# Performance work log

Measured on AMD Instinct MI355X. Metric: run time of the kernel, lower is better.

The kernel has to match this reference:

```python
import jax, jax.numpy as jnp
import numpy as np

N, E, F_IN, HID, HEADS, NCLS = 50000, 800000, 500, 16, 8, 40
NEG_SLOPE = 0.2


def setup_inputs() -> dict:
    key = jax.random.key(0)
    ks = jax.random.split(key, 10)
    x = jax.random.normal(ks[0], (N, F_IN), jnp.float32)
    edge_index = jax.random.randint(ks[1], (2, E), 0, N)
    W1 = jax.random.normal(ks[2], (F_IN, HEADS * HID), jnp.float32) * (1.0 / np.sqrt(F_IN))
    a_src1 = jax.random.normal(ks[3], (HEADS, HID), jnp.float32) * 0.1
    a_dst1 = jax.random.normal(ks[4], (HEADS, HID), jnp.float32) * 0.1
    b1 = jnp.zeros((HEADS * HID,), jnp.float32)
    W2 = jax.random.normal(ks[5], (HEADS * HID, NCLS), jnp.float32) * (1.0 / np.sqrt(HEADS * HID))
    a_src2 = jax.random.normal(ks[6], (1, NCLS), jnp.float32) * 0.1
    a_dst2 = jax.random.normal(ks[7], (1, NCLS), jnp.float32) * 0.1
    b2 = jnp.zeros((NCLS,), jnp.float32)
    return {"x": x, "edge_index": edge_index, "W1": W1, "a_src1": a_src1,
            "a_dst1": a_dst1, "b1": b1, "W2": W2, "a_src2": a_src2,
            "a_dst2": a_dst2, "b2": b2}


def gat_layer(x, edge_index, W, a_src, a_dst, b, heads, ch, concat):
    n = x.shape[0]
    h = (x @ W).reshape(n, heads, ch)                 # [N,H,C]
    alpha_src = jnp.sum(h * a_src, axis=-1)           # [N,H]
    alpha_dst = jnp.sum(h * a_dst, axis=-1)           # [N,H]
    loop = jnp.arange(n)                              # PyG add_self_loops=True
    src = jnp.concatenate([edge_index[0], loop])
    dst = jnp.concatenate([edge_index[1], loop])
    e = jax.nn.leaky_relu(alpha_src[src] + alpha_dst[dst], NEG_SLOPE)  # [E',H]
    # segment softmax over destination nodes
    m = jax.ops.segment_max(e, dst, num_segments=n)
    ex = jnp.exp(e - m[dst])
    denom = jax.ops.segment_sum(ex, dst, num_segments=n)
    alpha = ex / (denom[dst] + 1e-16)                 # [E',H]
    out = jax.ops.segment_sum(h[src] * alpha[:, :, None], dst, num_segments=n)  # [N,H,C]
    out = out.reshape(n, heads * ch) if concat else out.mean(axis=1)
    return out + b


def reference(x, edge_index, W1, a_src1, a_dst1, b1, W2, a_src2, a_dst2, b2):
    h = jax.nn.elu(gat_layer(x, edge_index, W1, a_src1, a_dst1, b1, HEADS, HID, True))
    # dropout p=0.6 is identity in eval mode
    h = gat_layer(h, edge_index, W2, a_src2, a_dst2, b2, 1, NCLS, False)
    return jax.nn.log_softmax(h, axis=1)
```

## Files before the change

### kernel.cpp

```cpp
#include <hip/hip_runtime.h>
#include <hip/hip_bf16.h>
#include <math.h>

#define N_NODES 50000
#define F_IN    500
#define HEADS   8
#define HID     16
#define HH      128
#define NCLS    40
#define NEG     0.2f

typedef _Float16 f16x2 __attribute__((ext_vector_type(2)));
typedef _Float16 f16x4 __attribute__((ext_vector_type(4)));
typedef _Float16 f16x8 __attribute__((ext_vector_type(8)));
typedef float    f32x4 __attribute__((ext_vector_type(4)));

__device__ __forceinline__ float lrelu(float x) { return x >= 0.f ? x : NEG * x; }

__global__ void convW_kernel(const float* __restrict__ W1, _Float16* __restrict__ Wt) {
    int i = blockIdx.x * 256 + threadIdx.x;
    if (i >= 128 * 512) return;
    int c = i >> 9, k = i & 511;
    Wt[i] = (k < F_IN) ? (_Float16)W1[k * HH + c] : (_Float16)0.f;
}

#define LDPB 136
__global__ __launch_bounds__(256) void gemm1_mfma(const float* __restrict__ x,
                                                  const _Float16* __restrict__ Wt,
                                                  _Float16* __restrict__ h1h) {
    __shared__ _Float16 Bs[128 * LDPB];
    const int t = threadIdx.x;
    const int lane = t & 63, w = t >> 6;
    const int rowBase = blockIdx.x * 64;
    const int arow = rowBase + 16 * w + (lane & 15);
    const bool rowok = arow < N_NODES;
    const int klo = (lane >> 4) * 8;
    const float* xrow = x + (size_t)arow * F_IN;

    f32x4 acc[8];
#pragma unroll
    for (int n = 0; n < 8; ++n) acc[n] = (f32x4){0.f, 0.f, 0.f, 0.f};

    const int gb = t & 15, cb = t >> 4;

    float4 pa0[4], pa1[4];
#pragma unroll
    for (int ks = 0; ks < 4; ++ks) {
        int kk = ks * 32 + klo;
        pa0[ks] = (rowok && kk < F_IN)     ? *(const float4*)&xrow[kk]     : make_float4(0, 0, 0, 0);
        pa1[ks] = (rowok && kk + 4 < F_IN) ? *(const float4*)&xrow[kk + 4] : make_float4(0, 0, 0, 0);
    }

    for (int kt = 0; kt < 4; ++kt) {
#pragma unroll
        for (int p = 0; p < 8; ++p) {
            int c = cb + 16 * p;
            *(f16x8*)&Bs[c * LDPB + 8 * gb] = *(const f16x8*)&Wt[c * 512 + kt * 128 + 8 * gb];
        }
        __syncthreads();

        f16x8 afr[4];
#pragma unroll
        for (int ks = 0; ks < 4; ++ks) {
            float4 a0 = pa0[ks], a1 = pa1[ks];
            afr[ks] = (f16x8){(_Float16)a0.x, (_Float16)a0.y, (_Float16)a0.z, (_Float16)a0.w,
                              (_Float16)a1.x, (_Float16)a1.y, (_Float16)a1.z, (_Float16)a1.w};
        }
        if (kt < 3) {
#pragma unroll
            for (int ks = 0; ks < 4; ++ks) {
                int kk = (kt + 1) * 128 + ks * 32 + klo;
                pa0[ks] = (rowok && kk < F_IN)     ? *(const float4*)&xrow[kk]     : make_float4(0, 0, 0, 0);
                pa1[ks] = (rowok && kk + 4 < F_IN) ? *(const float4*)&xrow[kk + 4] : make_float4(0, 0, 0, 0);
            }
        }
#pragma unroll
        for (int ks = 0; ks < 4; ++ks) {
#pragma unroll
            for (int n = 0; n < 8; ++n) {
                f16x8 b = *(const f16x8*)&Bs[(16 * n + (lane & 15)) * LDPB + ks * 32 + klo];
                acc[n] = __builtin_amdgcn_mfma_f32_16x16x32_f16(afr[ks], b, acc[n], 0, 0, 0);
            }
        }
        __syncthreads();
    }
    const int colb = lane & 15, rq = lane >> 4;
#pragma unroll
    for (int n = 0; n < 8; ++n) {
#pragma unroll
        for (int r = 0; r < 4; ++r) {
            int grow = rowBase + 16 * w + rq * 4 + r;
            if (grow < N_NODES) h1h[(size_t)grow * HH + 16 * n + colb] = (_Float16)acc[n][r];
        }
    }
}

__global__ void alpha1_kernel(const _Float16* __restrict__ h1h,
                              const float* __restrict__ a_src,
                              const float* __restrict__ a_dst,
                              float* __restrict__ asrc, float* __restrict__ adst) {
    int idx = blockIdx.x * blockDim.x + threadIdx.x;
    if (idx >= N_NODES * HEADS) return;
    int n = idx >> 3, h = idx & 7;
    const f16x8* hp = (const f16x8*)&h1h[(size_t)n * HH + h * HID];
    float s = 0.f, d = 0.f;
#pragma unroll
    for (int c = 0; c < 2; ++c) {
        f16x8 hv = hp[c];
#pragma unroll
        for (int i = 0; i < 8; ++i) {
            float f = (float)hv[i];
            s += f * a_src[h * HID + c * 8 + i];
            d += f * a_dst[h * HID + c * 8 + i];
        }
    }
    asrc[idx] = s;
    adst[idx] = d;
}

__global__ void zero_int_kernel(int* __restrict__ p, int n) {
    int i = blockIdx.x * blockDim.x + threadIdx.x;
    if (i < n) p[i] = 0;
}

__global__ void count_kernel(const int* __restrict__ ei, int* __restrict__ deg,
                             int E, int EP) {
    int e = blockIdx.x * blockDim.x + threadIdx.x;
    if (e >= EP) return;
    int dst = (e < E) ? ei[E + e] : (e - E);
    atomicAdd(&deg[dst], 1);
}

__global__ __launch_bounds__(256) void scan1_kernel(const int* __restrict__ deg,
                                                    int* __restrict__ offs,
                                                    int* __restrict__ bsums, int n) {
    __shared__ int sm[256];
    int tid = threadIdx.x, i = blockIdx.x * 256 + tid;
    int v = (i < n) ? deg[i] : 0;
    sm[tid] = v;
    __syncthreads();
    for (int off = 1; off < 256; off <<= 1) {
        int t = 0;
        if (tid >= off) t = sm[tid - off];
        __syncthreads();
        if (tid >= off) sm[tid] += t;
        __syncthreads();
    }
    if (i < n) offs[i] = sm[tid] - v;
    if (tid == 255) bsums[blockIdx.x] = sm[255];
}

__global__ __launch_bounds__(256) void scan2_kernel(const int* __restrict__ bsums,
                                                    int* __restrict__ boffs, int nb,
                                                    int* __restrict__ offs, int n) {
    __shared__ int sm[256];
    int tid = threadIdx.x;
    int v = (tid < nb) ? bsums[tid] : 0;
    sm[tid] = v;
    __syncthreads();
    for (int off = 1; off < 256; off <<= 1) {
        int t = 0;
        if (tid >= off) t = sm[tid - off];
        __syncthreads();
        if (tid >= off) sm[tid] += t;
        __syncthreads();
    }
    if (tid < nb) boffs[tid] = sm[tid] - v;
    if (tid == 255) offs[n] = sm[255];
}

__global__ __launch_bounds__(256) void scan3_kernel(int* __restrict__ offs,
                                                    int* __restrict__ cursor,
                                                    const int* __restrict__ boffs, int n) {
    int i = blockIdx.x * 256 + threadIdx.x;
    if (i >= n) return;
    int o = offs[i] + boffs[blockIdx.x];
    offs[i] = o;
    cursor[i] = o;
}

__global__ void fill_kernel(const int* __restrict__ ei, int* __restrict__ cursor,
                            int* __restrict__ bsrc, int E, int EP) {
    int e = blockIdx.x * blockDim.x + threadIdx.x;
    if (e >= EP) return;
    int src, dst;
    if (e < E) { src = ei[e]; dst = ei[E + e]; }
    else       { src = e - E; dst = e - E; }
    int slot = atomicAdd(&cursor[dst], 1);
    bsrc[slot] = src;
}

__global__ __launch_bounds__(256) void agg1_kernel(const _Float16* __restrict__ h1h,
                                                   const float* __restrict__ asrc,
                                                   const float* __restrict__ adst,
                                                   const int* __restrict__ offs,
                                                   const int* __restrict__ bsrc,
                                                   const float* __restrict__ b1,
                                                   _Float16* __restrict__ h1bh) {
    int lane = threadIdx.x & 63;
    int node = blockIdx.x * 4 + (threadIdx.x >> 6);
    if (node >= N_NODES) return;
    int beg = offs[node], end = offs[node + 1];
    int hh = lane >> 3;
    float adv = adst[node * 8 + hh];

    float acc0 = 0.f, acc1 = 0.f, dsum = 0.f;
    int j = beg;
    for (; j + 2 <= end; j += 2) {
        int s0 = bsrc[j], s1 = bsrc[j + 1];
        float sa0 = asrc[s0 * 8 + hh];
        float sa1 = asrc[s1 * 8 + hh];
        f16x2 hv0 = *(const f16x2*)&h1h[(size_t)s0 * HH + 2 * lane];
        f16x2 hv1 = *(const f16x2*)&h1h[(size_t)s1 * HH + 2 * lane];
        float w0 = __expf(lrelu(sa0 + adv));
        float w1 = __expf(lrelu(sa1 + adv));
        dsum += w0 + w1;
        acc0 += w0 * (float)hv0[0] + w1 * (float)hv1[0];
        acc1 += w0 * (float)hv0[1] + w1 * (float)hv1[1];
    }
    if (j < end) {
        int s0 = bsrc[j];
        float sa0 = asrc[s0 * 8 + hh];
        f16x2 hv0 = *(const f16x2*)&h1h[(size_t)s0 * HH + 2 * lane];
        float w0 = __expf(lrelu(sa0 + adv));
        dsum += w0;
        acc0 += w0 * (float)hv0[0];
        acc1 += w0 * (float)hv0[1];
    }
    float rv = 1.f / (dsum + 1e-16f);
    float2 bv = *(const float2*)&b1[2 * lane];
    float v0 = acc0 * rv + bv.x;
    float v1 = acc1 * rv + bv.y;
    v0 = v0 > 0.f ? v0 : __expf(v0) - 1.f;
    v1 = v1 > 0.f ? v1 : __expf(v1) - 1.f;
    f16x2 o = {(_Float16)v0, (_Float16)v1};
    *(f16x2*)&h1bh[(size_t)node * HH + 2 * lane] = o;
}

__global__ __launch_bounds__(256) void gemm2_kernel(const _Float16* __restrict__ h1bh,
                                                    const float* __restrict__ W2,
                                                    _Float16* __restrict__ h2h) {
    __shared__ float Ws[HH * NCLS];
    for (int i = threadIdx.x; i < HH * NCLS; i += 256) Ws[i] = W2[i];
    __syncthreads();
    int idx = blockIdx.x * 256 + threadIdx.x;
    if (idx >= N_NODES * NCLS) return;
    int n = idx / NCLS, c = idx - n * NCLS;
    const f16x8* hp = (const f16x8*)&h1bh[(size_t)n * HH];
    float acc = 0.f;
#pragma unroll
    for (int k8 = 0; k8 < HH / 8; ++k8) {
        f16x8 hv = hp[k8];
#pragma unroll
        for (int i = 0; i < 8; ++i)
            acc += (float)hv[i] * Ws[(k8 * 8 + i) * NCLS + c];
    }
    h2h[idx] = (_Float16)acc;
}

__global__ void alpha2_kernel(const _Float16* __restrict__ h2h,
                              const float* __restrict__ a_src,
                              const float* __restrict__ a_dst,
                              float* __restrict__ asrc, float* __restrict__ adst) {
    int n = blockIdx.x * blockDim.x + threadIdx.x;
    if (n >= N_NODES) return;
    const f16x8* hp = (const f16x8*)&h2h[(size_t)n * NCLS];
    float s = 0.f, d = 0.f;
#pragma unroll
    for (int c8 = 0; c8 < NCLS / 8; ++c8) {
        f16x8 hv = hp[c8];
#pragma unroll
        for (int i = 0; i < 8; ++i) {
            float f = (float)hv[i];
            s += f * a_src[c8 * 8 + i];
            d += f * a_dst[c8 * 8 + i];
        }
    }
    asrc[n] = s;
    adst[n] = d;
}

__global__ __launch_bounds__(256) void agg2_kernel(const _Float16* __restrict__ h2h,
                                                   const float* __restrict__ asrc,
                                                   const float* __restrict__ adst,
                                                   const int* __restrict__ offs,
                                                   const int* __restrict__ bsrc,
                                                   const float* __restrict__ b2,
                                                   float* __restrict__ out) {
    int lane = threadIdx.x & 63;
    int node = blockIdx.x * 4 + (threadIdx.x >> 6);
    if (node >= N_NODES) return;
    int beg = offs[node], end = offs[node + 1];
    float adv = adst[node];
    bool act = lane < NCLS / 2;

    float acc0 = 0.f, acc1 = 0.f, dsum = 0.f;
    int j = beg;
    for (; j + 2 <= end; j += 2) {
        int s0 = bsrc[j], s1 = bsrc[j + 1];
        float w0 = __expf(lrelu(asrc[s0] + adv));
        float w1 = __expf(lrelu(asrc[s1] + adv));
        f16x2 hv0 = {(_Float16)0.f, (_Float16)0.f}, hv1 = hv0;
        if (act) {
            hv0 = *(const f16x2*)&h2h[(size_t)s0 * NCLS + 2 * lane];
            hv1 = *(const f16x2*)&h2h[(size_t)s1 * NCLS + 2 * lane];
        }
        dsum += w0 + w1;
        acc0 += w0 * (float)hv0[0] + w1 * (float)hv1[0];
        acc1 += w0 * (float)hv0[1] + w1 * (float)hv1[1];
    }
    if (j < end) {
        int s0 = bsrc[j];
        float w0 = __expf(lrelu(asrc[s0] + adv));
        f16x2 hv0 = {(_Float16)0.f, (_Float16)0.f};
        if (act) hv0 = *(const f16x2*)&h2h[(size_t)s0 * NCLS + 2 * lane];
        dsum += w0;
        acc0 += w0 * (float)hv0[0];
        acc1 += w0 * (float)hv0[1];
    }
    float rd = 1.f / (dsum + 1e-16f);
    float v0 = -1e30f, v1 = -1e30f;
    if (act) {
        float2 bv = *(const float2*)&b2[2 * lane];
        v0 = acc0 * rd + bv.x;
        v1 = acc1 * rd + bv.y;
    }
    float m = fmaxf(v0, v1);
#pragma unroll
    for (int o = 32; o; o >>= 1) m = fmaxf(m, __shfl_xor(m, o, 64));
    float p = act ? (__expf(v0 - m) + __expf(v1 - m)) : 0.f;
#pragma unroll
    for (int o = 32; o; o >>= 1) p += __shfl_xor(p, o, 64);
    float ls = m + __logf(p);
    if (act) {
        float2 ov = make_float2(v0 - ls, v1 - ls);
        *(float2*)&out[(size_t)node * NCLS + 2 * lane] = ov;
    }
}

extern "C" void kernel_launch(void* const* d_in, const int* in_sizes, int n_in,
                              void* d_out, int out_size, void* d_ws, size_t ws_size,
                              hipStream_t stream) {
    const float* x      = (const float*)d_in[0];
    const int*   ei     = (const int*)d_in[1];
    const float* W1     = (const float*)d_in[2];
    const float* a_src1 = (const float*)d_in[3];
    const float* a_dst1 = (const float*)d_in[4];
    const float* b1     = (const float*)d_in[5];
    const float* W2     = (const float*)d_in[6];
    const float* a_src2 = (const float*)d_in[7];
    const float* a_dst2 = (const float*)d_in[8];
    const float* b2     = (const float*)d_in[9];
    float* out = (float*)d_out;

    const int E  = in_sizes[1] / 2;
    const int EP = E + N_NODES;
    const int NB = (N_NODES + 255) / 256;

    char* w = (char*)d_ws;
    _Float16* h1h   = (_Float16*)(w + 0);
    _Float16* h1bh  = (_Float16*)(w + 12800000);
    float*    asrc1 = (float*)(w + 25600000);
    float*    adst1 = (float*)(w + 27200000);
    _Float16* h2h   = (_Float16*)(w + 28800000);
    float*    asrc2 = (float*)(w + 32800000);
    float*    adst2 = (float*)(w + 33000000);
    int*      deg   = (int*)(w + 33200000);
    int*      offs  = (int*)(w + 33400064);
    int*      cursor= (int*)(w + 33600128);
    int*      bsrc  = (int*)(w + 33800192);
    _Float16* Wt    = (_Float16*)(w + 37200256);
    int*      bsums = (int*)(w + 37331328);
    int*      boffs = (int*)(w + 37332352);

    zero_int_kernel<<<(N_NODES + 255) / 256, 256, 0, stream>>>(deg, N_NODES);
    convW_kernel<<<(128 * 512 + 255) / 256, 256, 0, stream>>>(W1, Wt);
    gemm1_mfma<<<(N_NODES + 63) / 64, 256, 0, stream>>>(x, Wt, h1h);
    alpha1_kernel<<<(N_NODES * HEADS + 255) / 256, 256, 0, stream>>>(h1h, a_src1, a_dst1,
                                                                     asrc1, adst1);
    count_kernel<<<(EP + 255) / 256, 256, 0, stream>>>(ei, deg, E, EP);
    scan1_kernel<<<NB, 256, 0, stream>>>(deg, offs, bsums, N_NODES);
    scan2_kernel<<<1, 256, 0, stream>>>(bsums, boffs, NB, offs, N_NODES);
    scan3_kernel<<<NB, 256, 0, stream>>>(offs, cursor, boffs, N_NODES);
    fill_kernel<<<(EP + 255) / 256, 256, 0, stream>>>(ei, cursor, bsrc, E, EP);
    agg1_kernel<<<(N_NODES + 3) / 4, 256, 0, stream>>>(h1h, asrc1, adst1, offs, bsrc, b1, h1bh);
    gemm2_kernel<<<(N_NODES * NCLS + 255) / 256, 256, 0, stream>>>(h1bh, W2, h2h);
    alpha2_kernel<<<(N_NODES + 255) / 256, 256, 0, stream>>>(h2h, a_src2, a_dst2,
                                                             asrc2, adst2);
    agg2_kernel<<<(N_NODES + 3) / 4, 256, 0, stream>>>(h2h, asrc2, adst2, offs, bsrc, b2, out);
}
```

Measured before the change: 442.5 us.

## Fuse layer-2 GEMM with attention logits, deepen prefetch, unroll aggregation loops

The layer-2 projection and its attention-coefficient computation are merged into one wave-per-node kernel that reads a pre-transposed W2 and reduces the logits with shuffles, so the separate alpha2 launch and its re-read of h2 go away. The GEMM1 A-operand prefetch becomes double-buffered two k-tiles ahead, and both aggregation loops are unrolled to four edges to put more gathers in flight. The degree zeroing uses a memset, and the W1 and W2 transposes share one prep kernel. The new GEMM2 has each lane read a full 128-float W2t row from global memory instead of shared memory, and the deeper prefetch raises register use.

```diff
diff --git a/kernel.cpp b/kernel.cpp
--- a/kernel.cpp
+++ b/kernel.cpp
@@ -17,14 +17,22 @@
 
 __device__ __forceinline__ float lrelu(float x) { return x >= 0.f ? x : NEG * x; }
 
-__global__ void convW_kernel(const float* __restrict__ W1, _Float16* __restrict__ Wt) {
+__global__ void prep_kernel(const float* __restrict__ W1, const float* __restrict__ W2,
+                            _Float16* __restrict__ Wt, float* __restrict__ W2t) {
     int i = blockIdx.x * 256 + threadIdx.x;
-    if (i >= 128 * 512) return;
-    int c = i >> 9, k = i & 511;
-    Wt[i] = (k < F_IN) ? (_Float16)W1[k * HH + c] : (_Float16)0.f;
+    if (i < 128 * 512) {
+        int c = i >> 9, k = i & 511;
+        Wt[i] = (k < F_IN) ? (_Float16)W1[k * HH + c] : (_Float16)0.f;
+    }
+    int j = i - 128 * 512;
+    if (j >= 0 && j < 64 * HH) {
+        int c = j >> 7, k = j & 127;
+        W2t[j] = (c < NCLS) ? W2[k * NCLS + c] : 0.f;
+    }
 }
 
 #define LDPB 136
+
 __global__ __launch_bounds__(256) void gemm1_mfma(const float* __restrict__ x,
                                                   const _Float16* __restrict__ Wt,
                                                   _Float16* __restrict__ h1h) {
@@ -43,47 +51,61 @@
 
     const int gb = t & 15, cb = t >> 4;
 
-    float4 pa0[4], pa1[4];
-#pragma unroll
-    for (int ks = 0; ks < 4; ++ks) {
-        int kk = ks * 32 + klo;
-        pa0[ks] = (rowok && kk < F_IN)     ? *(const float4*)&xrow[kk]     : make_float4(0, 0, 0, 0);
-        pa1[ks] = (rowok && kk + 4 < F_IN) ? *(const float4*)&xrow[kk + 4] : make_float4(0, 0, 0, 0);
-    }
-
-    for (int kt = 0; kt < 4; ++kt) {
-#pragma unroll
-        for (int p = 0; p < 8; ++p) {
-            int c = cb + 16 * p;
-            *(f16x8*)&Bs[c * LDPB + 8 * gb] = *(const f16x8*)&Wt[c * 512 + kt * 128 + 8 * gb];
-        }
-        __syncthreads();
-
-        f16x8 afr[4];
-#pragma unroll
-        for (int ks = 0; ks < 4; ++ks) {
-            float4 a0 = pa0[ks], a1 = pa1[ks];
-            afr[ks] = (f16x8){(_Float16)a0.x, (_Float16)a0.y, (_Float16)a0.z, (_Float16)a0.w,
-                              (_Float16)a1.x, (_Float16)a1.y, (_Float16)a1.z, (_Float16)a1.w};
-        }
-        if (kt < 3) {
-#pragma unroll
-            for (int ks = 0; ks < 4; ++ks) {
-                int kk = (kt + 1) * 128 + ks * 32 + klo;
-                pa0[ks] = (rowok && kk < F_IN)     ? *(const float4*)&xrow[kk]     : make_float4(0, 0, 0, 0);
-                pa1[ks] = (rowok && kk + 4 < F_IN) ? *(const float4*)&xrow[kk + 4] : make_float4(0, 0, 0, 0);
-            }
-        }
-#pragma unroll
-        for (int ks = 0; ks < 4; ++ks) {
-#pragma unroll
-            for (int n = 0; n < 8; ++n) {
-                f16x8 b = *(const f16x8*)&Bs[(16 * n + (lane & 15)) * LDPB + ks * 32 + klo];
-                acc[n] = __builtin_amdgcn_mfma_f32_16x16x32_f16(afr[ks], b, acc[n], 0, 0, 0);
-            }
-        }
-        __syncthreads();
-    }
+    float4 A0[8], A1[8];
+
+#define LOADA(DST, KT)                                                              \
+    {                                                                               \
+        _Pragma("unroll")                                                           \
+        for (int ks = 0; ks < 4; ++ks) {                                            \
+            int kk = (KT) * 128 + ks * 32 + klo;                                    \
+            DST[2 * ks]     = (rowok && kk < F_IN)     ? *(const float4*)&xrow[kk]  \
+                                                       : make_float4(0, 0, 0, 0);   \
+            DST[2 * ks + 1] = (rowok && kk + 4 < F_IN) ? *(const float4*)&xrow[kk + 4] \
+                                                       : make_float4(0, 0, 0, 0);   \
+        }                                                                           \
+    }
+
+#define GSTEP(KT, CUR, DOPREF)                                                      \
+    {                                                                               \
+        _Pragma("unroll")                                                           \
+        for (int p = 0; p < 8; ++p) {                                               \
+            int c = cb + 16 * p;                                                    \
+            *(f16x8*)&Bs[c * LDPB + 8 * gb] =                                       \
+                *(const f16x8*)&Wt[c * 512 + (KT) * 128 + 8 * gb];                  \
+        }                                                                           \
+        __syncthreads();                                                            \
+        f16x8 afr[4];                                                               \
+        _Pragma("unroll")                                                           \
+        for (int ks = 0; ks < 4; ++ks) {                                            \
+            float4 a0 = CUR[2 * ks], a1 = CUR[2 * ks + 1];                          \
+            afr[ks] = (f16x8){(_Float16)a0.x, (_Float16)a0.y, (_Float16)a0.z,       \
+                              (_Float16)a0.w, (_Float16)a1.x, (_Float16)a1.y,       \
+                              (_Float16)a1.z, (_Float16)a1.w};                      \
+        }                                                                           \
+        if (DOPREF) LOADA(CUR, (KT) + 2);                                           \
+        _Pragma("unroll")                                                           \
+        for (int ks = 0; ks < 4; ++ks) {                                            \
+            _Pragma("unroll")                                                       \
+            for (int n = 0; n < 8; ++n) {                                           \
+                f16x8 b = *(const f16x8*)&Bs[(16 * n + (lane & 15)) * LDPB +        \
+                                             ks * 32 + klo];                        \
+                acc[n] = __builtin_amdgcn_mfma_f32_16x16x32_f16(afr[ks], b,         \
+                                                                acc[n], 0, 0, 0);   \
+            }                                                                       \
+        }                                                                           \
+        __syncthreads();                                                            \
+    }
+
+    LOADA(A0, 0)
+    LOADA(A1, 1)
+    GSTEP(0, A0, true)
+    GSTEP(1, A1, true)
+    GSTEP(2, A0, false)
+    GSTEP(3, A1, false)
+
+#undef GSTEP
+#undef LOADA
+
     const int colb = lane & 15, rq = lane >> 4;
 #pragma unroll
     for (int n = 0; n < 8; ++n) {
@@ -116,11 +138,6 @@
     }
     asrc[idx] = s;
     adst[idx] = d;
-}
-
-__global__ void zero_int_kernel(int* __restrict__ p, int n) {
-    int i = blockIdx.x * blockDim.x + threadIdx.x;
-    if (i < n) p[i] = 0;
 }
 
 __global__ void count_kernel(const int* __restrict__ ei, int* __restrict__ deg,
@@ -206,26 +223,30 @@
 
     float acc0 = 0.f, acc1 = 0.f, dsum = 0.f;
     int j = beg;
-    for (; j + 2 <= end; j += 2) {
-        int s0 = bsrc[j], s1 = bsrc[j + 1];
-        float sa0 = asrc[s0 * 8 + hh];
-        float sa1 = asrc[s1 * 8 + hh];
-        f16x2 hv0 = *(const f16x2*)&h1h[(size_t)s0 * HH + 2 * lane];
-        f16x2 hv1 = *(const f16x2*)&h1h[(size_t)s1 * HH + 2 * lane];
-        float w0 = __expf(lrelu(sa0 + adv));
-        float w1 = __expf(lrelu(sa1 + adv));
-        dsum += w0 + w1;
-        acc0 += w0 * (float)hv0[0] + w1 * (float)hv1[0];
-        acc1 += w0 * (float)hv0[1] + w1 * (float)hv1[1];
-    }
-    if (j < end) {
+    for (; j + 4 <= end; j += 4) {
+        int s0 = bsrc[j], s1 = bsrc[j + 1], s2 = bsrc[j + 2], s3 = bsrc[j + 3];
+        float a0 = asrc[s0 * 8 + hh], a1 = asrc[s1 * 8 + hh];
+        float a2 = asrc[s2 * 8 + hh], a3 = asrc[s3 * 8 + hh];
+        f16x2 h0 = *(const f16x2*)&h1h[(size_t)s0 * HH + 2 * lane];
+        f16x2 h1 = *(const f16x2*)&h1h[(size_t)s1 * HH + 2 * lane];
+        f16x2 h2 = *(const f16x2*)&h1h[(size_t)s2 * HH + 2 * lane];
+        f16x2 h3 = *(const f16x2*)&h1h[(size_t)s3 * HH + 2 * lane];
+        float w0 = __expf(lrelu(a0 + adv));
+        float w1 = __expf(lrelu(a1 + adv));
+        float w2 = __expf(lrelu(a2 + adv));
+        float w3 = __expf(lrelu(a3 + adv));
+        dsum += (w0 + w1) + (w2 + w3);
+        acc0 += w0 * (float)h0[0] + w1 * (float)h1[0] + w2 * (float)h2[0] + w3 * (float)h3[0];
+        acc1 += w0 * (float)h0[1] + w1 * (float)h1[1] + w2 * (float)h2[1] + w3 * (float)h3[1];
+    }
+    for (; j < end; ++j) {
         int s0 = bsrc[j];
-        float sa0 = asrc[s0 * 8 + hh];
-        f16x2 hv0 = *(const f16x2*)&h1h[(size_t)s0 * HH + 2 * lane];
-        float w0 = __expf(lrelu(sa0 + adv));
+        float a0 = asrc[s0 * 8 + hh];
+        f16x2 h0 = *(const f16x2*)&h1h[(size_t)s0 * HH + 2 * lane];
+        float w0 = __expf(lrelu(a0 + adv));
         dsum += w0;
-        acc0 += w0 * (float)hv0[0];
-        acc1 += w0 * (float)hv0[1];
+        acc0 += w0 * (float)h0[0];
+        acc1 += w0 * (float)h0[1];
     }
     float rv = 1.f / (dsum + 1e-16f);
     float2 bv = *(const float2*)&b1[2 * lane];
@@ -237,47 +258,39 @@
     *(f16x2*)&h1bh[(size_t)node * HH + 2 * lane] = o;
 }
 
-__global__ __launch_bounds__(256) void gemm2_kernel(const _Float16* __restrict__ h1bh,
-                                                    const float* __restrict__ W2,
-                                                    _Float16* __restrict__ h2h) {
-    __shared__ float Ws[HH * NCLS];
-    for (int i = threadIdx.x; i < HH * NCLS; i += 256) Ws[i] = W2[i];
-    __syncthreads();
-    int idx = blockIdx.x * 256 + threadIdx.x;
-    if (idx >= N_NODES * NCLS) return;
-    int n = idx / NCLS, c = idx - n * NCLS;
-    const f16x8* hp = (const f16x8*)&h1bh[(size_t)n * HH];
+__global__ __launch_bounds__(256) void gemm2b_kernel(const _Float16* __restrict__ h1bh,
+                                                     const float* __restrict__ W2t,
+                                                     const float* __restrict__ a_src2,
+                                                     const float* __restrict__ a_dst2,
+                                                     _Float16* __restrict__ h2h,
+                                                     float* __restrict__ asrc2,
+                                                     float* __restrict__ adst2) {
+    int lane = threadIdx.x & 63;
+    int node = blockIdx.x * 4 + (threadIdx.x >> 6);
+    if (node >= N_NODES) return;
+    const f16x8* hp = (const f16x8*)&h1bh[(size_t)node * HH];
+    const float* wrow = W2t + lane * HH;
     float acc = 0.f;
 #pragma unroll
-    for (int k8 = 0; k8 < HH / 8; ++k8) {
-        f16x8 hv = hp[k8];
-#pragma unroll
-        for (int i = 0; i < 8; ++i)
-            acc += (float)hv[i] * Ws[(k8 * 8 + i) * NCLS + c];
-    }
-    h2h[idx] = (_Float16)acc;
-}
-
-__global__ void alpha2_kernel(const _Float16* __restrict__ h2h,
-                              const float* __restrict__ a_src,
-                              const float* __restrict__ a_dst,
-                              float* __restrict__ asrc, float* __restrict__ adst) {
-    int n = blockIdx.x * blockDim.x + threadIdx.x;
-    if (n >= N_NODES) return;
-    const f16x8* hp = (const f16x8*)&h2h[(size_t)n * NCLS];
-    float s = 0.f, d = 0.f;
-#pragma unroll
-    for (int c8 = 0; c8 < NCLS / 8; ++c8) {
-        f16x8 hv = hp[c8];
-#pragma unroll
-        for (int i = 0; i < 8; ++i) {
-            float f = (float)hv[i];
-            s += f * a_src[c8 * 8 + i];
-            d += f * a_dst[c8 * 8 + i];
-        }
-    }
-    asrc[n] = s;
-    adst[n] = d;
+    for (int i = 0; i < 16; ++i) {
+        f16x8 hv = hp[i];
+#pragma unroll
+        for (int q = 0; q < 8; ++q)
+            acc += (float)hv[q] * wrow[i * 8 + q];
+    }
+    bool act = lane < NCLS;
+    if (act) h2h[(size_t)node * NCLS + lane] = (_Float16)acc;
+    float ps = act ? acc * a_src2[lane] : 0.f;
+    float pd = act ? acc * a_dst2[lane] : 0.f;
+#pragma unroll
+    for (int o = 32; o; o >>= 1) {
+        ps += __shfl_xor(ps, o, 64);
+        pd += __shfl_xor(pd, o, 64);
+    }
+    if (lane == 0) {
+        asrc2[node] = ps;
+        adst2[node] = pd;
+    }
 }
 
 __global__ __launch_bounds__(256) void agg2_kernel(const _Float16* __restrict__ h2h,
@@ -296,27 +309,31 @@
 
     float acc0 = 0.f, acc1 = 0.f, dsum = 0.f;
     int j = beg;
-    for (; j + 2 <= end; j += 2) {
-        int s0 = bsrc[j], s1 = bsrc[j + 1];
+    for (; j + 4 <= end; j += 4) {
+        int s0 = bsrc[j], s1 = bsrc[j + 1], s2 = bsrc[j + 2], s3 = bsrc[j + 3];
         float w0 = __expf(lrelu(asrc[s0] + adv));
         float w1 = __expf(lrelu(asrc[s1] + adv));
-        f16x2 hv0 = {(_Float16)0.f, (_Float16)0.f}, hv1 = hv0;
+        float w2 = __expf(lrelu(asrc[s2] + adv));
+        float w3 = __expf(lrelu(asrc[s3] + adv));
+        f16x2 h0 = {(_Float16)0.f, (_Float16)0.f}, h1 = h0, h2 = h0, h3 = h0;
         if (act) {
-            hv0 = *(const f16x2*)&h2h[(size_t)s0 * NCLS + 2 * lane];
-            hv1 = *(const f16x2*)&h2h[(size_t)s1 * NCLS + 2 * lane];
+            h0 = *(const f16x2*)&h2h[(size_t)s0 * NCLS + 2 * lane];
+            h1 = *(const f16x2*)&h2h[(size_t)s1 * NCLS + 2 * lane];
+            h2 = *(const f16x2*)&h2h[(size_t)s2 * NCLS + 2 * lane];
+            h3 = *(const f16x2*)&h2h[(size_t)s3 * NCLS + 2 * lane];
         }
-        dsum += w0 + w1;
-        acc0 += w0 * (float)hv0[0] + w1 * (float)hv1[0];
-        acc1 += w0 * (float)hv0[1] + w1 * (float)hv1[1];
-    }
-    if (j < end) {
+        dsum += (w0 + w1) + (w2 + w3);
+        acc0 += w0 * (float)h0[0] + w1 * (float)h1[0] + w2 * (float)h2[0] + w3 * (float)h3[0];
+        acc1 += w0 * (float)h0[1] + w1 * (float)h1[1] + w2 * (float)h2[1] + w3 * (float)h3[1];
+    }
+    for (; j < end; ++j) {
         int s0 = bsrc[j];
         float w0 = __expf(lrelu(asrc[s0] + adv));
-        f16x2 hv0 = {(_Float16)0.f, (_Float16)0.f};
-        if (act) hv0 = *(const f16x2*)&h2h[(size_t)s0 * NCLS + 2 * lane];
+        f16x2 h0 = {(_Float16)0.f, (_Float16)0.f};
+        if (act) h0 = *(const f16x2*)&h2h[(size_t)s0 * NCLS + 2 * lane];
         dsum += w0;
-        acc0 += w0 * (float)hv0[0];
-        acc1 += w0 * (float)hv0[1];
+        acc0 += w0 * (float)h0[0];
+        acc1 += w0 * (float)h0[1];
     }
     float rd = 1.f / (dsum + 1e-16f);
     float v0 = -1e30f, v1 = -1e30f;
@@ -372,9 +389,10 @@
     _Float16* Wt    = (_Float16*)(w + 37200256);
     int*      bsums = (int*)(w + 37331328);
     int*      boffs = (int*)(w + 37332352);
-
-    zero_int_kernel<<<(N_NODES + 255) / 256, 256, 0, stream>>>(deg, N_NODES);
-    convW_kernel<<<(128 * 512 + 255) / 256, 256, 0, stream>>>(W1, Wt);
+    float*    W2t   = (float*)(w + 37333376);
+
+    hipMemsetAsync(deg, 0, N_NODES * sizeof(int), stream);
+    prep_kernel<<<(128 * 512 + 64 * HH + 255) / 256, 256, 0, stream>>>(W1, W2, Wt, W2t);
     gemm1_mfma<<<(N_NODES + 63) / 64, 256, 0, stream>>>(x, Wt, h1h);
     alpha1_kernel<<<(N_NODES * HEADS + 255) / 256, 256, 0, stream>>>(h1h, a_src1, a_dst1,
                                                                      asrc1, adst1);
@@ -384,8 +402,7 @@
     scan3_kernel<<<NB, 256, 0, stream>>>(offs, cursor, boffs, N_NODES);
     fill_kernel<<<(EP + 255) / 256, 256, 0, stream>>>(ei, cursor, bsrc, E, EP);
     agg1_kernel<<<(N_NODES + 3) / 4, 256, 0, stream>>>(h1h, asrc1, adst1, offs, bsrc, b1, h1bh);
-    gemm2_kernel<<<(N_NODES * NCLS + 255) / 256, 256, 0, stream>>>(h1bh, W2, h2h);
-    alpha2_kernel<<<(N_NODES + 255) / 256, 256, 0, stream>>>(h2h, a_src2, a_dst2,
-                                                             asrc2, adst2);
+    gemm2b_kernel<<<(N_NODES + 3) / 4, 256, 0, stream>>>(h1bh, W2t, a_src2, a_dst2,
+                                                         h2h, asrc2, adst2);
     agg2_kernel<<<(N_NODES + 3) / 4, 256, 0, stream>>>(h2h, asrc2, adst2, offs, bsrc, b2, out);
 }
```

After: 589.8 us. 1.33x slower.
